# Performance work log

Measured on AMD Instinct MI355X. Metric: run time of the kernel, lower is better.

The kernel has to match this reference:

```python
import jax, jax.numpy as jnp
import numpy as np

HID = 128
CDIM = 128
NCH = 3
NDIM = 3


def _linear_params(key, fan_in, fan_out):
    kw, kb = jax.random.split(key)
    bound = 1.0 / np.sqrt(fan_in)
    W = jax.random.uniform(kw, (fan_in, fan_out), jnp.float32, -bound, bound)
    b = jax.random.uniform(kb, (fan_out,), jnp.float32, -bound, bound)
    return W, b


def setup_inputs() -> dict:
    key = jax.random.key(0)
    keys = jax.random.split(key, 12)
    p = jax.random.normal(keys[0], (32, 8192, NDIM), jnp.float32)
    W_pos, b_pos = _linear_params(keys[1], NDIM, 2 * HID)
    W0, b0 = _linear_params(keys[2], 2 * HID, HID)
    W1, b1 = _linear_params(keys[3], 2 * HID, HID)
    W2, b2 = _linear_params(keys[4], 2 * HID, HID)
    W3, b3 = _linear_params(keys[5], 2 * HID, HID)
    Wc, bc = _linear_params(keys[6], HID, CDIM)
    Wm0, bm0 = _linear_params(keys[7], CDIM, HID)
    Wm1, bm1 = _linear_params(keys[8], HID, HID)
    Wm2, bm2 = _linear_params(keys[9], HID, HID)
    Wp, bp = _linear_params(keys[10], HID, NCH * 3)
    return dict(p=p, W_pos=W_pos, b_pos=b_pos, W0=W0, b0=b0, W1=W1, b1=b1,
                W2=W2, b2=b2, W3=W3, b3=b3, Wc=Wc, bc=bc,
                Wm0=Wm0, bm0=bm0, Wm1=Wm1, bm1=bm1, Wm2=Wm2, bm2=bm2,
                Wp=Wp, bp=bp)


def _relu(x):
    return jnp.maximum(x, 0)


def _pool_cat(net):
    # max over points (dim=1), broadcast back and concat on features
    pooled = jnp.max(net, axis=1, keepdims=True)
    pooled = jnp.broadcast_to(pooled, net.shape)
    return jnp.concatenate([net, pooled], axis=2)  # [B, T, 2*hid]


def reference(p, W_pos, b_pos, W0, b0, W1, b1, W2, b2, W3, b3,
              Wc, bc, Wm0, bm0, Wm1, bm1, Wm2, bm2, Wp, bp):
    net = p @ W_pos + b_pos                      # [B, T, 2*hid]
    net = _relu(net) @ W0 + b0                   # [B, T, hid]
    net = _relu(_pool_cat(net)) @ W1 + b1        # [B, T, hid]
    net = _relu(_pool_cat(net)) @ W2 + b2        # [B, T, hid]
    net = _relu(_pool_cat(net)) @ W3 + b3        # [B, T, hid]
    net = jnp.max(net, axis=1)                   # [B, hid]
    net = _relu(net) @ Wc + bc                   # [B, c_dim]
    net = _relu(net) @ Wm0 + bm0
    net = _relu(net) @ Wm1 + bm1
    net = _relu(net) @ Wm2 + bm2
    net = _relu(net) @ Wp + bp                   # [B, n_channels*3]
    return net
```

## Files before the change

kernel.cpp:

```cpp
#include <hip/hip_runtime.h>


using bf16x8 = __attribute__((ext_vector_type(8))) __bf16;
using u16x8  = __attribute__((ext_vector_type(8))) unsigned short;
using f32x4  = __attribute__((ext_vector_type(4))) float;

__device__ __forceinline__ unsigned short f2bf(float x) {
  __bf16 b = (__bf16)x;
  return __builtin_bit_cast(unsigned short, b);
}

__device__ __forceinline__ f32x4 mfma16(bf16x8 a, bf16x8 b, f32x4 c) {
  return __builtin_amdgcn_mfma_f32_16x16x32_bf16(a, b, c, 0, 0, 0);
}

union FragU { unsigned short us[8]; u16x8 u; bf16x8 v; };

__global__ __launch_bounds__(256) void k_pack_all(
    const float* __restrict__ W0, const float* __restrict__ W1,
    const float* __restrict__ W2, const float* __restrict__ W3,
    unsigned short* __restrict__ Wt) {
  const int blk = blockIdx.x, t = threadIdx.x;
  const float* src; int slot; unsigned short* dst;
  if (blk < 16)      { src = W0; slot = blk * 256 + t;        dst = Wt; }
  else if (blk < 24) { src = W1; slot = (blk - 16) * 256 + t; dst = Wt + 32768; }
  else if (blk < 32) { src = W2; slot = (blk - 24) * 256 + t; dst = Wt + 49152; }
  else               { src = W3; slot = (blk - 32) * 256 + t; dst = Wt + 65536; }
  const int ks = slot >> 9, rem = slot & 511;
  const int nt = rem >> 6, lane = rem & 63;
  const int n = nt * 16 + (lane & 15);
  const int kb = ks * 32 + ((lane >> 4) << 3);
  FragU fr;
#pragma unroll
  for (int j = 0; j < 8; ++j) fr.us[j] = f2bf(src[(kb + j) * 128 + n]);
  reinterpret_cast<u16x8*>(dst)[slot] = fr.u;
}

__device__ __forceinline__ void epilogue512(
    unsigned short* hsw, float (*pmaxs)[128], const f32x4 (&acc)[2][8],
    const float (&bias)[8], int t, int blk, unsigned short* __restrict__ h,
    float* __restrict__ pm, bool write_h) {
  const int w = t >> 6, lane = t & 63, g = lane >> 4, c = lane & 15;
  float colmax[8];
#pragma unroll
  for (int nt = 0; nt < 8; ++nt) colmax[nt] = 0.f;

  if (write_h) {
    u16x8* hout = reinterpret_cast<u16x8*>(h) + (size_t)blk * 4096;
#pragma unroll
    for (int mi = 0; mi < 2; ++mi) {
#pragma unroll
      for (int nt = 0; nt < 8; ++nt) {
#pragma unroll
        for (int r = 0; r < 4; ++r) {
          const float v = fmaxf(acc[mi][nt][r] + bias[nt], 0.f);
          colmax[nt] = fmaxf(colmax[nt], v);
          hsw[(g * 4 + r) * 136 + nt * 16 + c] = f2bf(v);
        }
      }
#pragma unroll
      for (int s = 0; s < 4; ++s) {
        const u16x8 val =
            *reinterpret_cast<const u16x8*>(&hsw[(lane & 15) * 136 + s * 32 + 8 * g]);
        hout[(w * 2 + mi) * 256 + s * 64 + lane] = val;
      }
    }
  } else {
#pragma unroll
    for (int mi = 0; mi < 2; ++mi)
#pragma unroll
      for (int nt = 0; nt < 8; ++nt)
#pragma unroll
        for (int r = 0; r < 4; ++r)
          colmax[nt] = fmaxf(colmax[nt], acc[mi][nt][r] + bias[nt]);
  }

#pragma unroll
  for (int nt = 0; nt < 8; ++nt) {
    colmax[nt] = fmaxf(colmax[nt], __shfl_xor(colmax[nt], 16, 64));
    colmax[nt] = fmaxf(colmax[nt], __shfl_xor(colmax[nt], 32, 64));
  }
  if (lane < 16) {
#pragma unroll
    for (int nt = 0; nt < 8; ++nt) pmaxs[w][nt * 16 + c] = colmax[nt];
  }
  __syncthreads();
  if (t < 128) {
    float m = pmaxs[0][t];
#pragma unroll
    for (int i = 1; i < 8; ++i) m = fmaxf(m, pmaxs[i][t]);
    pm[(size_t)blk * 128 + t] = m;
  }
}

__global__ __launch_bounds__(512, 4) void k_layer0(
    const float* __restrict__ p, const float* __restrict__ Wpos,
    const float* __restrict__ bpos, const float* __restrict__ b0,
    const unsigned short* __restrict__ Wt0, unsigned short* __restrict__ h,
    float* __restrict__ pm) {
  __shared__ float wls[1024];
  __shared__ unsigned short HS[8 * 2176];
  __shared__ float pmaxs[8][128];
  const int t = threadIdx.x, blk = blockIdx.x;
  for (int i = t; i < 1024; i += 512) wls[i] = (i < 768) ? Wpos[i] : bpos[i - 768];

  const int w = t >> 6, lane = t & 63, g = lane >> 4, c = lane & 15;
  float px[2], py[2], pz[2];
#pragma unroll
  for (int mi = 0; mi < 2; ++mi) {
    const int row = blk * 256 + (w * 2 + mi) * 16 + c;
    px[mi] = p[row * 3 + 0]; py[mi] = p[row * 3 + 1]; pz[mi] = p[row * 3 + 2];
  }
  float bias[8];
#pragma unroll
  for (int nt = 0; nt < 8; ++nt) bias[nt] = b0[nt * 16 + c];

  f32x4 acc[2][8];
#pragma unroll
  for (int mi = 0; mi < 2; ++mi)
#pragma unroll
    for (int nt = 0; nt < 8; ++nt) acc[mi][nt] = f32x4{0.f, 0.f, 0.f, 0.f};
  __syncthreads();

  const bf16x8* Bf = reinterpret_cast<const bf16x8*>(Wt0);
#pragma unroll
  for (int ks = 0; ks < 8; ++ks) {
    FragU a[2];
    const int kb = ks * 32 + g * 8;
#pragma unroll
    for (int mi = 0; mi < 2; ++mi) {
#pragma unroll
      for (int half = 0; half < 2; ++half) {
        const int kq = kb + half * 4;
        const float4 w0 = *reinterpret_cast<const float4*>(&wls[kq]);
        const float4 w1 = *reinterpret_cast<const float4*>(&wls[256 + kq]);
        const float4 w2 = *reinterpret_cast<const float4*>(&wls[512 + kq]);
        const float4 bb = *reinterpret_cast<const float4*>(&wls[768 + kq]);
        a[mi].us[half * 4 + 0] = f2bf(fmaxf(bb.x + px[mi] * w0.x + py[mi] * w1.x + pz[mi] * w2.x, 0.f));
        a[mi].us[half * 4 + 1] = f2bf(fmaxf(bb.y + px[mi] * w0.y + py[mi] * w1.y + pz[mi] * w2.y, 0.f));
        a[mi].us[half * 4 + 2] = f2bf(fmaxf(bb.z + px[mi] * w0.z + py[mi] * w1.z + pz[mi] * w2.z, 0.f));
        a[mi].us[half * 4 + 3] = f2bf(fmaxf(bb.w + px[mi] * w0.w + py[mi] * w1.w + pz[mi] * w2.w, 0.f));
      }
    }
#pragma unroll
    for (int nt = 0; nt < 8; ++nt) {
      const bf16x8 B = Bf[(ks * 8 + nt) * 64 + lane];
      acc[0][nt] = mfma16(a[0].v, B, acc[0][nt]);
      acc[1][nt] = mfma16(a[1].v, B, acc[1][nt]);
    }
  }
  epilogue512(&HS[w * 2176], pmaxs, acc, bias, t, blk, h, pm, true);
}

__global__ __launch_bounds__(512, 4) void k_layer(
    const unsigned short* __restrict__ Wta, const float* __restrict__ cvec,
    unsigned short* __restrict__ h, float* __restrict__ pm, int write_h) {
  __shared__ unsigned short HS[8 * 2176];
  __shared__ float pmaxs[8][128];
  const int t = threadIdx.x, blk = blockIdx.x;
  const int w = t >> 6, lane = t & 63, c = lane & 15;
  const int b = blk >> 5;

  float bias[8];
#pragma unroll
  for (int nt = 0; nt < 8; ++nt) bias[nt] = cvec[b * 128 + nt * 16 + c];

  f32x4 acc[2][8];
#pragma unroll
  for (int mi = 0; mi < 2; ++mi)
#pragma unroll
    for (int nt = 0; nt < 8; ++nt) acc[mi][nt] = f32x4{0.f, 0.f, 0.f, 0.f};

  const u16x8* hbase = reinterpret_cast<const u16x8*>(h) + (size_t)blk * 4096;
  const bf16x8* Bf = reinterpret_cast<const bf16x8*>(Wta);
#pragma unroll
  for (int ks = 0; ks < 4; ++ks) {
    FragU a0, a1;
    a0.u = hbase[(w * 2 + 0) * 256 + ks * 64 + lane];
    a1.u = hbase[(w * 2 + 1) * 256 + ks * 64 + lane];
#pragma unroll
    for (int nt = 0; nt < 8; ++nt) {
      const bf16x8 B = Bf[(ks * 8 + nt) * 64 + lane];
      acc[0][nt] = mfma16(a0.v, B, acc[0][nt]);
      acc[1][nt] = mfma16(a1.v, B, acc[1][nt]);
    }
  }
  epilogue512(&HS[w * 2176], pmaxs, acc, bias, t, blk, h, pm, write_h != 0);
}

__global__ __launch_bounds__(256) void k_combine(
    const float* __restrict__ pm, const float* __restrict__ Wn,
    const float* __restrict__ bn, float* __restrict__ cout) {
  const int b = blockIdx.x, t = threadIdx.x;
  const int f = t & 127, half = t >> 7;
  __shared__ float part[2][128];
  __shared__ float rm[128];
  float m = 0.f;
  for (int i = half * 16; i < half * 16 + 16; ++i)
    m = fmaxf(m, pm[(size_t)(b * 32 + i) * 128 + f]);
  part[half][f] = m;
  __syncthreads();
  if (t < 128) rm[f] = fmaxf(part[0][f], part[1][f]);
  __syncthreads();
  float s = 0.f;
  for (int q = half * 64; q < half * 64 + 64; ++q)
    s += rm[q] * Wn[(128 + q) * 128 + f];
  part[half][f] = s;
  __syncthreads();
  if (t < 128) cout[b * 128 + f] = part[0][f] + part[1][f] + bn[f];
}

__global__ __launch_bounds__(256) void k_final(
    const float* __restrict__ pm3,
    const float* __restrict__ Wc,  const float* __restrict__ bc,
    const float* __restrict__ Wm0, const float* __restrict__ bm0,
    const float* __restrict__ Wm1, const float* __restrict__ bm1,
    const float* __restrict__ Wm2, const float* __restrict__ bm2,
    const float* __restrict__ Wp,  const float* __restrict__ bp,
    float* __restrict__ out) {
  const int b = blockIdx.x, t = threadIdx.x;
  const int f = t & 127, half = t >> 7;
  __shared__ float part[2][128];
  __shared__ float x[128];
  float m = 0.f;
  for (int i = half * 16; i < half * 16 + 16; ++i)
    m = fmaxf(m, pm3[(size_t)(b * 32 + i) * 128 + f]);
  part[half][f] = m;
  __syncthreads();
  if (t < 128) x[f] = fmaxf(part[0][f], part[1][f]);
  __syncthreads();

  const float* Ws[4] = {Wc, Wm0, Wm1, Wm2};
  const float* bs[4] = {bc, bm0, bm1, bm2};
#pragma unroll
  for (int L = 0; L < 4; ++L) {
    float s = 0.f;
    for (int q = half * 64; q < half * 64 + 64; ++q)
      s += x[q] * Ws[L][q * 128 + f];
    part[half][f] = s;
    __syncthreads();
    if (t < 128) x[f] = fmaxf(part[0][f] + part[1][f] + bs[L][f], 0.f);
    __syncthreads();
  }
  if (t < 9) {
    float s = bp[t];
    for (int q = 0; q < 128; ++q) s += x[q] * Wp[q * 9 + t];
    out[b * 9 + t] = s;
  }
}

extern "C" void kernel_launch(void* const* d_in, const int* in_sizes, int n_in,
                              void* d_out, int out_size, void* d_ws, size_t ws_size,
                              hipStream_t stream) {
  const float *p = nullptr, *Wpos = nullptr, *bpos = nullptr;
  const float *Wp = nullptr, *bp = nullptr;
  const float *W256[4] = {}; int nW256 = 0;
  const float *W128[4] = {}; int nW128 = 0;
  const float *B128[8] = {}; int nB128 = 0;
  for (int i = 0; i < n_in; ++i) {
    const float* q = (const float*)d_in[i];
    switch (in_sizes[i]) {
      case 786432: p = q; break;
      case 768:    Wpos = q; break;
      case 256:    bpos = q; break;
      case 1152:   Wp = q; break;
      case 9:      bp = q; break;
      case 32768:  if (nW256 < 4) W256[nW256++] = q; break;
      case 16384:  if (nW128 < 4) W128[nW128++] = q; break;
      case 128:    if (nB128 < 8) B128[nB128++] = q; break;
      default: break;
    }
  }
  const float *W0 = W256[0], *W1 = W256[1], *W2 = W256[2], *W3 = W256[3];
  const float *Wc = W128[0], *Wm0 = W128[1], *Wm1 = W128[2], *Wm2 = W128[3];
  const float *b0 = B128[0], *b1 = B128[1], *b2 = B128[2], *b3 = B128[3];
  const float *bc = B128[4], *bm0 = B128[5], *bm1 = B128[6], *bm2 = B128[7];
  float* out = (float*)d_out;

  char* ws = (char*)d_ws;
  float* pm = (float*)ws;
  float* cv = (float*)(ws + 524288);
  unsigned short* Wt = (unsigned short*)(ws + 524288 + 16384);
  unsigned short* Wt0 = Wt;
  unsigned short* Wt1 = Wt + 32768;
  unsigned short* Wt2 = Wt + 49152;
  unsigned short* Wt3 = Wt + 65536;
  unsigned short* h = Wt + 81920;

  k_pack_all<<<40, 256, 0, stream>>>(W0, W1, W2, W3, Wt);
  k_layer0<<<1024, 512, 0, stream>>>(p, Wpos, bpos, b0, Wt0, h, pm);
  k_combine<<<32, 256, 0, stream>>>(pm, W1, b1, cv);
  k_layer<<<1024, 512, 0, stream>>>(Wt1, cv, h, pm, 1);
  k_combine<<<32, 256, 0, stream>>>(pm, W2, b2, cv);
  k_layer<<<1024, 512, 0, stream>>>(Wt2, cv, h, pm, 1);
  k_combine<<<32, 256, 0, stream>>>(pm, W3, b3, cv);
  k_layer<<<1024, 512, 0, stream>>>(Wt3, cv, h, pm, 0);
  k_final<<<32, 256, 0, stream>>>(pm, Wc, bc, Wm0, bm0, Wm1, bm1, Wm2, bm2, Wp, bp, out);
}
```

Before: 160.3 us.

## Swap MFMA operand order to write activations directly, removing LDS transpose

Swaps the A/B operands of the MFMA so accumulators hold transposed tiles (features along rows). The epilogue can then store bf16 activations straight to global memory in the packed fragment layout, with no shared-memory staging buffer. The column max becomes a cross-lane shuffle reduction over 16 lanes. This removes the LDS round trip and frees shared memory, at the cost of narrower 8-byte global stores and more shuffles.

New measurement: 181.6 us. 1.13x slower.

```diff
diff --git a/kernel.cpp b/kernel.cpp
--- a/kernel.cpp
+++ b/kernel.cpp
@@ -36,53 +36,43 @@
   reinterpret_cast<u16x8*>(dst)[slot] = fr.u;
 }
 
-__device__ __forceinline__ void epilogue512(
-    unsigned short* hsw, float (*pmaxs)[128], const f32x4 (&acc)[2][8],
-    const float (&bias)[8], int t, int blk, unsigned short* __restrict__ h,
-    float* __restrict__ pm, bool write_h) {
+__device__ __forceinline__ void epilogue_swapped(
+    float (*pmaxs)[128], const f32x4 (&acc)[2][8],
+    const float* __restrict__ biasvec, int t, int blk,
+    unsigned short* __restrict__ h, float* __restrict__ pm, bool write_h) {
   const int w = t >> 6, lane = t & 63, g = lane >> 4, c = lane & 15;
-  float colmax[8];
-#pragma unroll
-  for (int nt = 0; nt < 8; ++nt) colmax[nt] = 0.f;
-
-  if (write_h) {
-    u16x8* hout = reinterpret_cast<u16x8*>(h) + (size_t)blk * 4096;
+  unsigned short* hblk = h + (size_t)blk * 32768;
+#pragma unroll
+  for (int nt = 0; nt < 8; ++nt) {
+    const float4 bb = *reinterpret_cast<const float4*>(&biasvec[nt * 16 + g * 4]);
+    float vm[4] = {0.f, 0.f, 0.f, 0.f};
 #pragma unroll
     for (int mi = 0; mi < 2; ++mi) {
-#pragma unroll
-      for (int nt = 0; nt < 8; ++nt) {
-#pragma unroll
-        for (int r = 0; r < 4; ++r) {
-          const float v = fmaxf(acc[mi][nt][r] + bias[nt], 0.f);
-          colmax[nt] = fmaxf(colmax[nt], v);
-          hsw[(g * 4 + r) * 136 + nt * 16 + c] = f2bf(v);
-        }
+      const float v0 = fmaxf(acc[mi][nt][0] + bb.x, 0.f);
+      const float v1 = fmaxf(acc[mi][nt][1] + bb.y, 0.f);
+      const float v2 = fmaxf(acc[mi][nt][2] + bb.z, 0.f);
+      const float v3 = fmaxf(acc[mi][nt][3] + bb.w, 0.f);
+      vm[0] = fmaxf(vm[0], v0); vm[1] = fmaxf(vm[1], v1);
+      vm[2] = fmaxf(vm[2], v2); vm[3] = fmaxf(vm[3], v3);
+      if (write_h) {
+        ushort4 s4;
+        s4.x = f2bf(v0); s4.y = f2bf(v1); s4.z = f2bf(v2); s4.w = f2bf(v3);
+        const int slot = (w * 2 + mi) * 256 + (nt >> 1) * 64 +
+                         ((nt & 1) * 2 + (g >> 1)) * 16 + c;
+        *reinterpret_cast<ushort4*>(&hblk[slot * 8 + (g & 1) * 4]) = s4;
       }
-#pragma unroll
-      for (int s = 0; s < 4; ++s) {
-        const u16x8 val =
-            *reinterpret_cast<const u16x8*>(&hsw[(lane & 15) * 136 + s * 32 + 8 * g]);
-        hout[(w * 2 + mi) * 256 + s * 64 + lane] = val;
-      }
-    }
-  } else {
-#pragma unroll
-    for (int mi = 0; mi < 2; ++mi)
-#pragma unroll
-      for (int nt = 0; nt < 8; ++nt)
-#pragma unroll
-        for (int r = 0; r < 4; ++r)
-          colmax[nt] = fmaxf(colmax[nt], acc[mi][nt][r] + bias[nt]);
-  }
-
-#pragma unroll
-  for (int nt = 0; nt < 8; ++nt) {
-    colmax[nt] = fmaxf(colmax[nt], __shfl_xor(colmax[nt], 16, 64));
-    colmax[nt] = fmaxf(colmax[nt], __shfl_xor(colmax[nt], 32, 64));
-  }
-  if (lane < 16) {
-#pragma unroll
-    for (int nt = 0; nt < 8; ++nt) pmaxs[w][nt * 16 + c] = colmax[nt];
+    }
+#pragma unroll
+    for (int r = 0; r < 4; ++r) {
+      vm[r] = fmaxf(vm[r], __shfl_xor(vm[r], 1, 64));
+      vm[r] = fmaxf(vm[r], __shfl_xor(vm[r], 2, 64));
+      vm[r] = fmaxf(vm[r], __shfl_xor(vm[r], 4, 64));
+      vm[r] = fmaxf(vm[r], __shfl_xor(vm[r], 8, 64));
+    }
+    if (c == 0) {
+#pragma unroll
+      for (int r = 0; r < 4; ++r) pmaxs[w][nt * 16 + g * 4 + r] = vm[r];
+    }
   }
   __syncthreads();
   if (t < 128) {
@@ -99,7 +89,6 @@
     const unsigned short* __restrict__ Wt0, unsigned short* __restrict__ h,
     float* __restrict__ pm) {
   __shared__ float wls[1024];
-  __shared__ unsigned short HS[8 * 2176];
   __shared__ float pmaxs[8][128];
   const int t = threadIdx.x, blk = blockIdx.x;
   for (int i = t; i < 1024; i += 512) wls[i] = (i < 768) ? Wpos[i] : bpos[i - 768];
@@ -111,9 +100,6 @@
     const int row = blk * 256 + (w * 2 + mi) * 16 + c;
     px[mi] = p[row * 3 + 0]; py[mi] = p[row * 3 + 1]; pz[mi] = p[row * 3 + 2];
   }
-  float bias[8];
-#pragma unroll
-  for (int nt = 0; nt < 8; ++nt) bias[nt] = b0[nt * 16 + c];
 
   f32x4 acc[2][8];
 #pragma unroll
@@ -144,26 +130,21 @@
     }
 #pragma unroll
     for (int nt = 0; nt < 8; ++nt) {
-      const bf16x8 B = Bf[(ks * 8 + nt) * 64 + lane];
-      acc[0][nt] = mfma16(a[0].v, B, acc[0][nt]);
-      acc[1][nt] = mfma16(a[1].v, B, acc[1][nt]);
-    }
-  }
-  epilogue512(&HS[w * 2176], pmaxs, acc, bias, t, blk, h, pm, true);
+      const bf16x8 Wf = Bf[(ks * 8 + nt) * 64 + lane];
+      acc[0][nt] = mfma16(Wf, a[0].v, acc[0][nt]);
+      acc[1][nt] = mfma16(Wf, a[1].v, acc[1][nt]);
+    }
+  }
+  epilogue_swapped(pmaxs, acc, b0, t, blk, h, pm, true);
 }
 
 __global__ __launch_bounds__(512, 4) void k_layer(
     const unsigned short* __restrict__ Wta, const float* __restrict__ cvec,
     unsigned short* __restrict__ h, float* __restrict__ pm, int write_h) {
-  __shared__ unsigned short HS[8 * 2176];
   __shared__ float pmaxs[8][128];
   const int t = threadIdx.x, blk = blockIdx.x;
-  const int w = t >> 6, lane = t & 63, c = lane & 15;
+  const int w = t >> 6, lane = t & 63;
   const int b = blk >> 5;
-
-  float bias[8];
-#pragma unroll
-  for (int nt = 0; nt < 8; ++nt) bias[nt] = cvec[b * 128 + nt * 16 + c];
 
   f32x4 acc[2][8];
 #pragma unroll
@@ -180,12 +161,12 @@
     a1.u = hbase[(w * 2 + 1) * 256 + ks * 64 + lane];
 #pragma unroll
     for (int nt = 0; nt < 8; ++nt) {
-      const bf16x8 B = Bf[(ks * 8 + nt) * 64 + lane];
-      acc[0][nt] = mfma16(a0.v, B, acc[0][nt]);
-      acc[1][nt] = mfma16(a1.v, B, acc[1][nt]);
-    }
-  }
-  epilogue512(&HS[w * 2176], pmaxs, acc, bias, t, blk, h, pm, write_h != 0);
+      const bf16x8 Wf = Bf[(ks * 8 + nt) * 64 + lane];
+      acc[0][nt] = mfma16(Wf, a0.v, acc[0][nt]);
+      acc[1][nt] = mfma16(Wf, a1.v, acc[1][nt]);
+    }
+  }
+  epilogue_swapped(pmaxs, acc, cvec + b * 128, t, blk, h, pm, write_h != 0);
 }
 
 __global__ __launch_bounds__(256) void k_combine(
```
